# Kernel tuning notes

Measured on AMD Instinct MI355X. Metric: run time of the kernel, lower is better.

The kernel has to match this reference:

```python
import jax, jax.numpy as jnp
import numpy as np

B, T = 1, 1024
HID = 2048
H, HKV, D = 16, 4, 128
G = H // HKV          # kv groups
TOPK = 256
HI, DI = 4, 32        # indexer heads / head dim


def _rotate_half(x):
    x1, x2 = jnp.split(x, 2, axis=-1)
    return jnp.concatenate([-x2, x1], axis=-1)


def _apply_rotary(x, cos, sin):
    # x: (B,T,H,D), cos/sin: (1,T,1,D)
    return x * cos + _rotate_half(x) * sin


def _rms_norm(x):
    eps = jnp.finfo(x.dtype).eps
    return x * jax.lax.rsqrt(jnp.mean(x * x, axis=-1, keepdims=True) + eps)


def setup_inputs() -> dict:
    key = jax.random.key(0)
    ks = jax.random.split(key, 9)
    s = 0.02
    x = jax.random.normal(ks[0], (B, T, HID), jnp.float32)
    # rotary tables
    inv_freq = 1.0 / (10000.0 ** (jnp.arange(0, D, 2, dtype=jnp.float32) / D))
    freqs = jnp.outer(jnp.arange(T, dtype=jnp.float32), inv_freq)   # (T, D/2)
    emb = jnp.concatenate([freqs, freqs], axis=-1)                  # (T, D)
    cos = jnp.cos(emb)[None, :, None, :]
    sin = jnp.sin(emb)[None, :, None, :]
    Wq = jax.random.normal(ks[1], (HID, H * D), jnp.float32) * s
    Wk = jax.random.normal(ks[2], (HID, HKV * D), jnp.float32) * s
    Wv = jax.random.normal(ks[3], (HID, HKV * D), jnp.float32) * s
    Wo = jax.random.normal(ks[4], (H * D, HID), jnp.float32) * s
    Wqi = jax.random.normal(ks[5], (HID, HI * DI), jnp.float32) * s
    Wwi = jax.random.normal(ks[6], (HID, HI), jnp.float32) * s
    Wki = jax.random.normal(ks[7], (HID, DI), jnp.float32) * s
    return {"x": x, "cos": cos, "sin": sin, "Wq": Wq, "Wk": Wk, "Wv": Wv,
            "Wo": Wo, "Wqi": Wqi, "Wwi": Wwi, "Wki": Wki}


def reference(x, cos, sin, Wq, Wk, Wv, Wo, Wqi, Wwi, Wki):
    b, t, _ = x.shape
    q = (x @ Wq).reshape(b, t, H, D)
    k = (x @ Wk).reshape(b, t, HKV, D)
    v = (x @ Wv).reshape(b, t, HKV, D)
    q = _rms_norm(_apply_rotary(q, cos, sin))
    k = _rms_norm(_apply_rotary(k, cos, sin))

    # ---- lightning indexer: I[t,s] = sum_j w[t,j] * relu(q_i[t,j] . k_i[s]) ----
    qi = (x @ Wqi).reshape(b, t, HI, DI)
    wi = x @ Wwi                                   # (B,T,HI)
    ki = x @ Wki                                   # (B,T,DI)
    raw = jax.nn.relu(jnp.einsum('bthd,bsd->bths', qi, ki))
    idx_scores = jnp.einsum('bths,bth->bts', raw, wi)     # (B,T,T)

    pos = jnp.arange(t)
    causal = pos[None, :] <= pos[:, None]                 # (T,T) valid s<=t
    masked = jnp.where(causal[None], idx_scores, -jnp.inf)
    _, top_idx = jax.lax.top_k(masked, TOPK)              # (B,T,K) int32

    # gather selected K/V: (B,T,K,HKV,D)
    gather = jax.vmap(lambda arr, idx: arr[idx])          # per-batch fancy gather
    sel_k = gather(k, top_idx)
    sel_v = gather(v, top_idx)
    sel_mask = top_idx <= pos[None, :, None]              # (B,T,K)

    # grouped-query attention over selected tokens (avoid repeat_interleave)
    q5 = q.reshape(b, t, HKV, G, D)                       # q head h -> kv head h//G
    scale = D ** -0.5
    scores = jnp.einsum('btngd,btknd->btngk', q5, sel_k) * scale
    scores = jnp.where(sel_mask[:, :, None, None, :], scores, -jnp.inf)
    probs = jax.nn.softmax(scores, axis=-1)
    attn = jnp.einsum('btngk,btknd->btngd', probs, sel_v)  # (B,T,HKV,G,D)
    out = attn.reshape(b, t, H * D) @ Wo
    return out
```

## Files before the change

### kernel.cpp

```cpp
#include <hip/hip_runtime.h>
#include <hip/hip_bf16.h>
#include <math.h>

#define T_    1024
#define HID_  2048
#define NH    16
#define NKV   4
#define DH    128
#define TOPK_ 256
#define HI_   4
#define DI_   32
#define NPROJ 3072
#define NIDX  164
#define KSPLIT 8
#define KCHUNK 256

#ifndef INFINITY
#define INFINITY (__builtin_inff())
#endif

typedef __attribute__((ext_vector_type(8))) short bf16x8;
typedef __attribute__((ext_vector_type(4))) float f32x4;

__device__ inline unsigned int packbf(float f) {
    unsigned int u = __float_as_uint(f);
    return (u + 0x7fffu + ((u >> 16) & 1u)) >> 16;
}

#define GLDS16(g, l) __builtin_amdgcn_global_load_lds( \
    (const __attribute__((address_space(1))) void*)(g), \
    (__attribute__((address_space(3))) void*)(l), 16, 0, 0)

__device__ inline void tcast_body(const float* __restrict__ W, unsigned short* __restrict__ Wt,
                                  int N, int bx, int by, int tid, float (*tile)[33]) {
    const int n0 = bx * 32, k0 = by * 32;
    const int tx = tid & 31, ty = tid >> 5;
#pragma unroll
    for (int i = 0; i < 4; ++i)
        tile[ty + i * 8][tx] = W[(size_t)(k0 + ty + i * 8) * N + (n0 + tx)];
    __syncthreads();
#pragma unroll
    for (int i = 0; i < 4; ++i) {
        int n = n0 + ty + i * 8;
        Wt[(size_t)n * HID_ + k0 + tx] = (unsigned short)packbf(tile[tx][ty + i * 8]);
    }
}

__device__ inline void gemm64_body(const unsigned short* __restrict__ A,
                                   const unsigned short* __restrict__ Bt,
                                   float* __restrict__ C, int K, int ldc,
                                   int bx, int by, int tid,
                                   unsigned short* As, unsigned short* Bs) {
    const int lane = tid & 63, w = tid >> 6;
    const int wr = w >> 1, wc = w & 1;
    const int brow = by * 64, bcol = bx * 64;
    const int l15 = lane & 15, lq = lane >> 4;

    f32x4 acc[2][2] = {};

    const int srow = tid >> 3;
    const int gsrc = ((tid & 7) ^ (srow & 7)) * 8;
    const unsigned short* ga  = A  + (size_t)(brow + srow) * K + gsrc;
    const unsigned short* ga2 = ga + (size_t)32 * K;
    const unsigned short* gb  = Bt + (size_t)(bcol + srow) * K + gsrc;
    const unsigned short* gb2 = gb + (size_t)32 * K;
    const int lo1 = tid * 8, lo2 = (tid + 256) * 8;

    GLDS16(ga,  &As[lo1]);
    GLDS16(ga2, &As[lo2]);
    GLDS16(gb,  &Bs[lo1]);
    GLDS16(gb2, &Bs[lo2]);
    __syncthreads();

    const int NT = K >> 6;
    for (int kt = 0; kt < NT; ++kt) {
        const int cur = (kt & 1) * 4096;
        if (kt + 1 < NT) {
            const int nxt = ((kt + 1) & 1) * 4096;
            const int k0 = (kt + 1) << 6;
            GLDS16(ga + k0,  &As[nxt + lo1]);
            GLDS16(ga2 + k0, &As[nxt + lo2]);
            GLDS16(gb + k0,  &Bs[nxt + lo1]);
            GLDS16(gb2 + k0, &Bs[nxt + lo2]);
        }
        const unsigned short* Ac = &As[cur];
        const unsigned short* Bc = &Bs[cur];
        bf16x8 fa[2][2], fb[2][2];
#pragma unroll
        for (int m = 0; m < 2; ++m)
#pragma unroll
            for (int kk = 0; kk < 2; ++kk) {
                int row = wr * 32 + m * 16 + l15;
                fa[m][kk] = *(const bf16x8*)&Ac[row * 64 + (((kk * 4 + lq) ^ (l15 & 7)) * 8)];
            }
#pragma unroll
        for (int nn = 0; nn < 2; ++nn)
#pragma unroll
            for (int kk = 0; kk < 2; ++kk) {
                int row = wc * 32 + nn * 16 + l15;
                fb[nn][kk] = *(const bf16x8*)&Bc[row * 64 + (((kk * 4 + lq) ^ (l15 & 7)) * 8)];
            }
#pragma unroll
        for (int kk = 0; kk < 2; ++kk)
#pragma unroll
            for (int m = 0; m < 2; ++m)
#pragma unroll
                for (int nn = 0; nn < 2; ++nn)
                    acc[m][nn] = __builtin_amdgcn_mfma_f32_16x16x32_bf16(fa[m][kk], fb[nn][kk], acc[m][nn], 0, 0, 0);
        __syncthreads();
    }
#pragma unroll
    for (int m = 0; m < 2; ++m)
#pragma unroll
        for (int nn = 0; nn < 2; ++nn)
#pragma unroll
            for (int q = 0; q < 4; ++q) {
                int row = brow + wr * 32 + m * 16 + lq * 4 + q;
                int col = bcol + wc * 32 + nn * 16 + l15;
                C[(size_t)row * ldc + col] = acc[m][nn][q];
            }
}

__global__ __launch_bounds__(256) void prep1(const float* __restrict__ x,
                                             const float* __restrict__ Wq,
                                             const float* __restrict__ Wk,
                                             const float* __restrict__ Wv,
                                             const float* __restrict__ Wqi,
                                             const float* __restrict__ Wwi,
                                             const float* __restrict__ Wki,
                                             unsigned short* __restrict__ xb,
                                             unsigned short* __restrict__ WtAll,
                                             float* __restrict__ Wi) {
    __shared__ float tile[32][33];
    int bid = blockIdx.x;
    const int tid = threadIdx.x;
    if (bid < 4096) { tcast_body(Wq, WtAll, HID_, bid & 63, bid >> 6, tid, tile); return; }
    bid -= 4096;
    if (bid < 1024) { tcast_body(Wk, WtAll + (size_t)2048 * HID_, 512, bid & 15, bid >> 4, tid, tile); return; }
    bid -= 1024;
    if (bid < 1024) { tcast_body(Wv, WtAll + (size_t)2560 * HID_, 512, bid & 15, bid >> 4, tid, tile); return; }
    bid -= 1024;
    if (bid < 1024) {
        int e = bid * 256 + tid;
        const float4* p = (const float4*)(x + (size_t)e * 8);
        float4 a = p[0], b = p[1];
        uint4 r;
        r.x = packbf(a.x) | (packbf(a.y) << 16);
        r.y = packbf(a.z) | (packbf(a.w) << 16);
        r.z = packbf(b.x) | (packbf(b.y) << 16);
        r.w = packbf(b.z) | (packbf(b.w) << 16);
        *(uint4*)(xb + (size_t)e * 8) = r;
        return;
    }
    bid -= 1024;
    {
        int e = bid * 256 + tid;
        if (e >= HID_ * NIDX) return;
        int k = e / NIDX, c = e - k * NIDX;
        float v;
        if (c < 128) v = Wqi[(size_t)k * 128 + c];
        else if (c < 132) v = Wwi[(size_t)k * 4 + (c - 128)];
        else v = Wki[(size_t)k * 32 + (c - 132)];
        Wi[e] = v;
    }
}

__global__ __launch_bounds__(256) void fusedA(const unsigned short* __restrict__ xb,
                                              const unsigned short* __restrict__ WtAll,
                                              float* __restrict__ proj,
                                              const float* __restrict__ x,
                                              const float* __restrict__ Wi,
                                              float* __restrict__ Cpart,
                                              const float* __restrict__ Wo,
                                              unsigned short* __restrict__ Wot) {
    __shared__ __align__(16) char smem[64 * 64 * 2 * 2 * 2];
    const int tid = threadIdx.x;
    int bid = blockIdx.x;

    if (bid < 768) {
        unsigned short* As = (unsigned short*)smem;
        unsigned short* Bs = As + 8192;
        gemm64_body(xb, WtAll, proj, HID_, NPROJ, bid % 48, bid / 48, tid, As, Bs);
        return;
    }
    bid -= 768;
    if (bid < 384) {
        float (*As2)[68] = (float(*)[68])smem;
        float (*Bs2)[68] = As2 + 16;
        const int bx = bid % 3, by = (bid / 3) % 16, z = bid / 48;
        const int tx = tid & 15, ty = tid >> 4;
        const int brow = by * 64, bcol = bx * 64;
        const int kbeg = z * KCHUNK, kend = kbeg + KCHUNK;
        const int M = T_, N = NIDX, K = HID_;

        const int ar = tid >> 2, ac4 = (tid & 3) * 4;
        const int br = tid >> 4, bc4 = (tid & 15) * 4;

        float acc[4][4];
#pragma unroll
        for (int i = 0; i < 4; ++i)
#pragma unroll
            for (int j = 0; j < 4; ++j) acc[i][j] = 0.f;

        for (int k0 = kbeg; k0 < kend; k0 += 16) {
            float4 va = *(const float4*)&x[(size_t)(brow + ar) * K + k0 + ac4];
            float4 vb;
            int col = bcol + bc4;
            if (col <= N - 4) vb = *(const float4*)&Wi[(size_t)(k0 + br) * N + col];
            else vb = (float4){0.f, 0.f, 0.f, 0.f};
            As2[ac4 + 0][ar] = va.x;
            As2[ac4 + 1][ar] = va.y;
            As2[ac4 + 2][ar] = va.z;
            As2[ac4 + 3][ar] = va.w;
            *(float4*)&Bs2[br][bc4] = vb;
            __syncthreads();
#pragma unroll
            for (int kk = 0; kk < 16; ++kk) {
                float4 a4 = *(const float4*)&As2[kk][ty * 4];
                float4 b4 = *(const float4*)&Bs2[kk][tx * 4];
                float a[4] = {a4.x, a4.y, a4.z, a4.w};
                float b[4] = {b4.x, b4.y, b4.z, b4.w};
#pragma unroll
                for (int i = 0; i < 4; ++i)
#pragma unroll
                    for (int j = 0; j < 4; ++j) acc[i][j] += a[i] * b[j];
            }
            __syncthreads();
        }
#pragma unroll
        for (int i = 0; i < 4; ++i) {
            int r = brow + ty * 4 + i;
#pragma unroll
            for (int j = 0; j < 4; ++j) {
                int c = bcol + tx * 4 + j;
                if (c < NIDX) Cpart[((size_t)z * T_ + r) * NIDX + c] = acc[i][j];
            }
        }
        return;
    }
    bid -= 384;
    {
        float (*tile)[33] = (float(*)[33])smem;
        tcast_body(Wo, Wot, HID_, bid & 63, bid >> 6, tid, tile);
    }
}

__global__ __launch_bounds__(256) void reduce_k(const float* __restrict__ Cpart,
                                                float* __restrict__ Cout,
                                                float* __restrict__ kib, int MN) {
    int e = blockIdx.x * 256 + threadIdx.x;
    if (e >= MN) return;
    float s = 0.f;
#pragma unroll
    for (int z = 0; z < KSPLIT; ++z) s += Cpart[(size_t)z * MN + e];
    Cout[e] = s;
    int t = e / NIDX, c = e - t * NIDX;
    if (c >= 132) kib[(size_t)t * DI_ + (c - 132)] = s;
}

__global__ __launch_bounds__(256) void fusedB(const float* __restrict__ proj,
                                              const float* __restrict__ cosb,
                                              const float* __restrict__ sinb,
                                              unsigned short* __restrict__ qbb,
                                              unsigned short* __restrict__ kbb,
                                              unsigned int* __restrict__ vbb,
                                              const float* __restrict__ proji,
                                              const float* __restrict__ kib,
                                              int* __restrict__ idxout) {
    const int tid = threadIdx.x;
    int bid = blockIdx.x;

    if (bid < 1024) {
        const int t = bid;
        int* orow = idxout + (size_t)t * TOPK_;
        if (t < TOPK_) { orow[tid] = tid; return; }

        __shared__ float qsh[128];
        __shared__ float wsh[4];
        if (tid < 128) qsh[tid] = proji[(size_t)t * NIDX + tid];
        else if (tid < 132) wsh[tid - 128] = proji[(size_t)t * NIDX + tid];
        __syncthreads();

        const int n = t + 1;
        const int lane = tid & 63, wave = tid >> 6;

        unsigned int key[4];
#pragma unroll
        for (int j = 0; j < 4; ++j) {
            int s = j * 256 + tid;
            if (s < n) {
                const float4* kr = (const float4*)&kib[(size_t)s * DI_];
                float4 k4[8];
#pragma unroll
                for (int d4 = 0; d4 < 8; ++d4) k4[d4] = kr[d4];
                float sc = 0.f;
#pragma unroll
                for (int h = 0; h < HI_; ++h) {
                    float d = 0.f;
#pragma unroll
                    for (int d4 = 0; d4 < 8; ++d4) {
                        const float* qp = &qsh[h * 32 + d4 * 4];
                        d += k4[d4].x * qp[0] + k4[d4].y * qp[1] +
                             k4[d4].z * qp[2] + k4[d4].w * qp[3];
                    }
                    sc += wsh[h] * fmaxf(d, 0.f);
                }
                unsigned int u = __float_as_uint(sc);
                key[j] = (u & 0x80000000u) ? ~u : (u | 0x80000000u);
            } else key[j] = 0u;
        }

        __shared__ int wcnt[2][4];
        unsigned int prefix = 0;
#pragma unroll 1
        for (int b = 31; b >= 0; --b) {
            unsigned int cand = prefix | (1u << b);
            int c = (key[0] >= cand) + (key[1] >= cand) + (key[2] >= cand) + (key[3] >= cand);
#pragma unroll
            for (int o = 32; o > 0; o >>= 1) c += __shfl_xor(c, o);
            if (lane == 0) wcnt[b & 1][wave] = c;
            __syncthreads();
            int total = wcnt[b & 1][0] + wcnt[b & 1][1] + wcnt[b & 1][2] + wcnt[b & 1][3];
            if (total >= TOPK_) prefix = cand;
        }
        const unsigned int T = prefix;

        __shared__ int posc;
        __shared__ int eqtot[4][4];
        __syncthreads();
        {
            int c = (key[0] > T) + (key[1] > T) + (key[2] > T) + (key[3] > T);
#pragma unroll
            for (int o = 32; o > 0; o >>= 1) c += __shfl_xor(c, o);
            if (lane == 0) wcnt[0][wave] = c;
        }
        if (tid == 0) posc = 0;

        int e[4]; int myp[4];
#pragma unroll
        for (int j = 0; j < 4; ++j) {
            e[j] = (key[j] == T) ? 1 : 0;
            unsigned long long m = __ballot(e[j]);
            myp[j] = __popcll(m & ((1ull << lane) - 1ull));
            if (lane == 0) eqtot[j][wave] = __popcll(m);
        }
        __syncthreads();
        const int cntGT = wcnt[0][0] + wcnt[0][1] + wcnt[0][2] + wcnt[0][3];
        const int need = TOPK_ - cntGT;

#pragma unroll
        for (int j = 0; j < 4; ++j)
            if (key[j] > T) {
                int p = atomicAdd(&posc, 1);
                orow[p] = j * 256 + tid;
            }
        int runbase = 0;
#pragma unroll
        for (int j = 0; j < 4; ++j) {
            int wavebase = 0;
#pragma unroll
            for (int w2 = 0; w2 < 4; ++w2) if (w2 < wave) wavebase += eqtot[j][w2];
            int g = runbase + wavebase + myp[j];
            if (e[j] && g < need) orow[cntGT + g] = j * 256 + tid;
            runbase += eqtot[j][0] + eqtot[j][1] + eqtot[j][2] + eqtot[j][3];
        }
        return;
    }
    bid -= 1024;
    {
        const int w = tid >> 6, lane = tid & 63;
        const int u = bid * 4 + w;
        const int t = u / 21, h = u - t * 21;
        if (h < 20) {
            const float* row;
            unsigned short* dst;
            if (h < 16) { row = proj + (size_t)t * NPROJ + h * DH;               dst = qbb + ((size_t)t * NH + h) * DH; }
            else        { row = proj + (size_t)t * NPROJ + HID_ + (h - 16) * DH; dst = kbb + ((size_t)t * NKV + (h - 16)) * DH; }
            float a = row[lane], b = row[lane + 64];
            float c0 = cosb[t * DH + lane],      s0 = sinb[t * DH + lane];
            float c1 = cosb[t * DH + lane + 64], s1 = sinb[t * DH + lane + 64];
            float r0 = a * c0 - b * s0;
            float r1 = b * c1 + a * s1;
            float ss = r0 * r0 + r1 * r1;
#pragma unroll
            for (int o = 32; o > 0; o >>= 1) ss += __shfl_xor(ss, o);
            float inv = rsqrtf(ss * (1.0f / 128.0f) + 1.1920929e-07f);
            dst[lane]      = (unsigned short)packbf(r0 * inv);
            dst[lane + 64] = (unsigned short)packbf(r1 * inv);
        } else {
            const float* src = proj + (size_t)t * NPROJ + HID_ + 512;
#pragma unroll
            for (int i = 0; i < 4; ++i) {
                int c2 = lane + i * 64;
                vbb[(size_t)t * 256 + c2] = packbf(src[2 * c2]) | (packbf(src[2 * c2 + 1]) << 16);
            }
        }
    }
}

__global__ __launch_bounds__(256) void gemm64(const unsigned short* __restrict__ A,
                                              const unsigned short* __restrict__ Bt,
                                              float* __restrict__ C,
                                              int K, int ldc) {
    __shared__ unsigned short As[2 * 64 * 64];
    __shared__ unsigned short Bs[2 * 64 * 64];
    gemm64_body(A, Bt, C, K, ldc, blockIdx.x, blockIdx.y, threadIdx.x, As, Bs);
}

__global__ __launch_bounds__(256) void attn8(const unsigned short* __restrict__ qbb,
                                             const unsigned short* __restrict__ kbb,
                                             const unsigned short* __restrict__ vbb,
                                             const int* __restrict__ idx,
                                             unsigned short* __restrict__ attnb) {
    const int t = blockIdx.x, n = blockIdx.y;
    const int tid = threadIdx.x, lane = tid & 63, w = tid >> 6;
    const int C = (t + 1 < TOPK_) ? t + 1 : TOPK_;
    const int l15 = lane & 15, lq = lane >> 4;

    __shared__ int sidx[TOPK_];
    __shared__ float sp[4][TOPK_];
    __shared__ float sinv[4];
    __shared__ unsigned short P[4][264];
    __shared__ unsigned short Vs[2][32 * 128];

    sidx[tid] = idx[(size_t)t * TOPK_ + tid];
    __syncthreads();

#define STAGE_V(buf, tau)                                                          \
    {                                                                              \
        _Pragma("unroll")                                                          \
        for (int it = 0; it < 2; ++it) {                                           \
            int c = tid + it * 256;                                                \
            int r = c >> 4, doff = (c & 15) * 8;                                   \
            int gs = doff ^ (((r >> 3) & 3) << 4);                                 \
            GLDS16(&vbb[((size_t)sidx[(tau) * 32 + r] * NKV + n) * DH + gs],       \
                   &Vs[buf][(size_t)c * 8]);                                       \
        }                                                                          \
    }

    STAGE_V(0, 0);

    const size_t qrow = (size_t)t * NH + n * 4 + (l15 < 4 ? l15 : 3);
    bf16x8 qf[4];
#pragma unroll
    for (int ks = 0; ks < 4; ++ks)
        qf[ks] = *(const bf16x8*)&qbb[qrow * DH + ks * 32 + lq * 8];

    bf16x8 kf[4], kf2[4];
    {
        const unsigned short* kr0 = &kbb[((size_t)sidx[(w * 4) * 16 + l15] * NKV + n) * DH];
#pragma unroll
        for (int ks = 0; ks < 4; ++ks) kf[ks] = *(const bf16x8*)&kr0[ks * 32 + lq * 8];
    }
#pragma unroll
    for (int tt = 0; tt < 4; ++tt) {
        if (tt < 3) {
            const unsigned short* krn =
                &kbb[((size_t)sidx[(w * 4 + tt + 1) * 16 + l15] * NKV + n) * DH];
#pragma unroll
            for (int ks = 0; ks < 4; ++ks) kf2[ks] = *(const bf16x8*)&krn[ks * 32 + lq * 8];
        }
        f32x4 acc = {0.f, 0.f, 0.f, 0.f};
        __builtin_amdgcn_s_setprio(1);
#pragma unroll
        for (int ks = 0; ks < 4; ++ks)
            acc = __builtin_amdgcn_mfma_f32_16x16x32_bf16(qf[ks], kf[ks], acc, 0, 0, 0);
        __builtin_amdgcn_s_setprio(0);
        if (lane < 16) {
            int j = (w * 4 + tt) * 16 + lane;
            bool ok = j < C;
#pragma unroll
            for (int q = 0; q < 4; ++q)
                sp[q][j] = ok ? acc[q] * 0.08838834764831845f : -INFINITY;
        }
#pragma unroll
        for (int ks = 0; ks < 4; ++ks) kf[ks] = kf2[ks];
    }
    __syncthreads();

    {
        float v0 = sp[w][lane], v1 = sp[w][lane + 64],
              v2 = sp[w][lane + 128], v3 = sp[w][lane + 192];
        float m = fmaxf(fmaxf(v0, v1), fmaxf(v2, v3));
#pragma unroll
        for (int o = 32; o > 0; o >>= 1) m = fmaxf(m, __shfl_xor(m, o));
        float e0 = expf(v0 - m), e1 = expf(v1 - m), e2 = expf(v2 - m), e3 = expf(v3 - m);
        float sum = e0 + e1 + e2 + e3;
#pragma unroll
        for (int o = 32; o > 0; o >>= 1) sum += __shfl_xor(sum, o);
        if (lane == 0) sinv[w] = 1.f / sum;
        P[w][lane]       = (unsigned short)packbf(e0);
        P[w][lane + 64]  = (unsigned short)packbf(e1);
        P[w][lane + 128] = (unsigned short)packbf(e2);
        P[w][lane + 192] = (unsigned short)packbf(e3);
    }
    __syncthreads();

    const int prow = (l15 < 4) ? l15 : 3;
    f32x4 pacc[2] = {};
#pragma unroll
    for (int tau = 0; tau < 8; ++tau) {
        const unsigned short* Vb = Vs[tau & 1];
        if (tau < 7) STAGE_V((tau + 1) & 1, tau + 1);
        bf16x8 xf = *(const bf16x8*)&P[prow][tau * 32 + lq * 8];
        const int colr0 = ((2 * w + 0) * 16 + l15) ^ (lq << 4);
        const int colr1 = ((2 * w + 1) * 16 + l15) ^ (lq << 4);
        bf16x8 yf0, yf1;
#pragma unroll
        for (int j = 0; j < 8; ++j) {
            yf0[j] = (short)Vb[(lq * 8 + j) * 128 + colr0];
            yf1[j] = (short)Vb[(lq * 8 + j) * 128 + colr1];
        }
        __builtin_amdgcn_s_setprio(1);
        pacc[0] = __builtin_amdgcn_mfma_f32_16x16x32_bf16(xf, yf0, pacc[0], 0, 0, 0);
        pacc[1] = __builtin_amdgcn_mfma_f32_16x16x32_bf16(xf, yf1, pacc[1], 0, 0, 0);
        __builtin_amdgcn_s_setprio(0);
        __syncthreads();
    }
#undef STAGE_V

    if (lane < 16) {
#pragma unroll
        for (int dt = 0; dt < 2; ++dt)
#pragma unroll
            for (int q = 0; q < 4; ++q)
                attnb[(size_t)(t * NH + n * 4 + q) * DH + (2 * w + dt) * 16 + l15] =
                    (unsigned short)packbf(pacc[dt][q] * sinv[q]);
    }
}

extern "C" void kernel_launch(void* const* d_in, const int* in_sizes, int n_in,
                              void* d_out, int out_size, void* d_ws, size_t ws_size,
                              hipStream_t stream) {
    const float* x    = (const float*)d_in[0];
    const float* cosb = (const float*)d_in[1];
    const float* sinb = (const float*)d_in[2];
    const float* Wq   = (const float*)d_in[3];
    const float* Wk   = (const float*)d_in[4];
    const float* Wv   = (const float*)d_in[5];
    const float* Wo   = (const float*)d_in[6];
    const float* Wqi  = (const float*)d_in[7];
    const float* Wwi  = (const float*)d_in[8];
    const float* Wki  = (const float*)d_in[9];
    float* out = (float*)d_out;

    unsigned short* xb    = (unsigned short*)d_ws;
    unsigned short* WtAll = xb + 2097152;
    float*  proj  = (float*)(WtAll + 6291456);
    float*  Wi    = proj + 3145728;
    float*  proji = Wi + 335872;
    float*  kib   = proji + 167936;
    int*    idxb  = (int*)(kib + 1048576);
    unsigned short* kbb   = (unsigned short*)(idxb + 262144);
    unsigned short* vbb   = kbb + 524288;
    unsigned short* attnb = vbb + 524288;
    unsigned short* Wot   = attnb + 2097152;
    unsigned short* qbb   = xb;
    float* Cpart = (float*)kbb;

    prep1<<<dim3(8480), dim3(256), 0, stream>>>(x, Wq, Wk, Wv, Wqi, Wwi, Wki, xb, WtAll, Wi);

    fusedA<<<dim3(5248), dim3(256), 0, stream>>>(xb, WtAll, proj, x, Wi, Cpart, Wo, Wot);

    reduce_k<<<dim3((T_ * NIDX + 255) / 256), dim3(256), 0, stream>>>(Cpart, proji, kib, T_ * NIDX);

    fusedB<<<dim3(6400), dim3(256), 0, stream>>>(proj, cosb, sinb, qbb, kbb, (unsigned int*)vbb,
                                                 proji, kib, idxb);

    attn8<<<dim3(T_, NKV), dim3(256), 0, stream>>>(qbb, kbb, vbb, idxb, attnb);

    gemm64<<<dim3(HID_ / 64, T_ / 64), dim3(256), 0, stream>>>(attnb, Wot, out, HID_, HID_);
}
```

Before: 151.5 us.

## Split sparse attention over top-k halves with separate softmax combine kernel

Each (token, kv-head) attention block is split into two blocks that each process 128 of the 256 selected keys. Each block writes unnormalized fp32 partial outputs plus per-head max and sum. A new combine kernel merges the halves with log-sum-exp rescaling and writes bf16 output. This doubles parallelism and halves the serial per-block work, at the cost of an extra launch and extra global traffic for the fp32 partials.

```diff
diff --git a/kernel.cpp b/kernel.cpp
--- a/kernel.cpp
+++ b/kernel.cpp
@@ -191,7 +191,7 @@
         const int tx = tid & 15, ty = tid >> 4;
         const int brow = by * 64, bcol = bx * 64;
         const int kbeg = z * KCHUNK, kend = kbeg + KCHUNK;
-        const int M = T_, N = NIDX, K = HID_;
+        const int N = NIDX, K = HID_;
 
         const int ar = tid >> 2, ac4 = (tid & 3) * 4;
         const int br = tid >> 4, bc4 = (tid & 15) * 4;
@@ -407,23 +407,25 @@
     gemm64_body(A, Bt, C, K, ldc, blockIdx.x, blockIdx.y, threadIdx.x, As, Bs);
 }
 
-__global__ __launch_bounds__(256) void attn8(const unsigned short* __restrict__ qbb,
+__global__ __launch_bounds__(256) void attn9(const unsigned short* __restrict__ qbb,
                                              const unsigned short* __restrict__ kbb,
                                              const unsigned short* __restrict__ vbb,
                                              const int* __restrict__ idx,
-                                             unsigned short* __restrict__ attnb) {
-    const int t = blockIdx.x, n = blockIdx.y;
+                                             float* __restrict__ Opart,
+                                             float* __restrict__ mlbuf) {
+    const int t = blockIdx.x;
+    const int n = blockIdx.y >> 1, half = blockIdx.y & 1;
     const int tid = threadIdx.x, lane = tid & 63, w = tid >> 6;
     const int C = (t + 1 < TOPK_) ? t + 1 : TOPK_;
     const int l15 = lane & 15, lq = lane >> 4;
-
-    __shared__ int sidx[TOPK_];
-    __shared__ float sp[4][TOPK_];
-    __shared__ float sinv[4];
-    __shared__ unsigned short P[4][264];
+    const size_t ob = (((size_t)t * NKV + n) * 2 + half) * 4;
+
+    __shared__ int sidx[128];
+    __shared__ float sp[4][128];
+    __shared__ unsigned short P[4][136];
     __shared__ unsigned short Vs[2][32 * 128];
 
-    sidx[tid] = idx[(size_t)t * TOPK_ + tid];
+    if (tid < 128) sidx[tid] = idx[(size_t)t * TOPK_ + half * 128 + tid];
     __syncthreads();
 
 #define STAGE_V(buf, tau)                                                          \
@@ -448,15 +450,15 @@
 
     bf16x8 kf[4], kf2[4];
     {
-        const unsigned short* kr0 = &kbb[((size_t)sidx[(w * 4) * 16 + l15] * NKV + n) * DH];
+        const unsigned short* kr0 = &kbb[((size_t)sidx[(w * 2) * 16 + l15] * NKV + n) * DH];
 #pragma unroll
         for (int ks = 0; ks < 4; ++ks) kf[ks] = *(const bf16x8*)&kr0[ks * 32 + lq * 8];
     }
 #pragma unroll
-    for (int tt = 0; tt < 4; ++tt) {
-        if (tt < 3) {
+    for (int tt = 0; tt < 2; ++tt) {
+        if (tt < 1) {
             const unsigned short* krn =
-                &kbb[((size_t)sidx[(w * 4 + tt + 1) * 16 + l15] * NKV + n) * DH];
+                &kbb[((size_t)sidx[(w * 2 + 1) * 16 + l15] * NKV + n) * DH];
 #pragma unroll
             for (int ks = 0; ks < 4; ++ks) kf2[ks] = *(const bf16x8*)&krn[ks * 32 + lq * 8];
         }
@@ -467,11 +469,11 @@
             acc = __builtin_amdgcn_mfma_f32_16x16x32_bf16(qf[ks], kf[ks], acc, 0, 0, 0);
         __builtin_amdgcn_s_setprio(0);
         if (lane < 16) {
-            int j = (w * 4 + tt) * 16 + lane;
-            bool ok = j < C;
+            int jl = (w * 2 + tt) * 16 + lane;
+            bool ok = (half * 128 + jl) < C;
 #pragma unroll
             for (int q = 0; q < 4; ++q)
-                sp[q][j] = ok ? acc[q] * 0.08838834764831845f : -INFINITY;
+                sp[q][jl] = ok ? acc[q] * 0.08838834764831845f : -INFINITY;
         }
 #pragma unroll
         for (int ks = 0; ks < 4; ++ks) kf[ks] = kf2[ks];
@@ -479,29 +481,30 @@
     __syncthreads();
 
     {
-        float v0 = sp[w][lane], v1 = sp[w][lane + 64],
-              v2 = sp[w][lane + 128], v3 = sp[w][lane + 192];
-        float m = fmaxf(fmaxf(v0, v1), fmaxf(v2, v3));
+        float v0 = sp[w][lane], v1 = sp[w][lane + 64];
+        float m = fmaxf(v0, v1);
 #pragma unroll
         for (int o = 32; o > 0; o >>= 1) m = fmaxf(m, __shfl_xor(m, o));
-        float e0 = expf(v0 - m), e1 = expf(v1 - m), e2 = expf(v2 - m), e3 = expf(v3 - m);
-        float sum = e0 + e1 + e2 + e3;
+        float mg = (m == -INFINITY) ? 0.f : m;
+        float e0 = expf(v0 - mg), e1 = expf(v1 - mg);
+        float sum = e0 + e1;
 #pragma unroll
         for (int o = 32; o > 0; o >>= 1) sum += __shfl_xor(sum, o);
-        if (lane == 0) sinv[w] = 1.f / sum;
-        P[w][lane]       = (unsigned short)packbf(e0);
-        P[w][lane + 64]  = (unsigned short)packbf(e1);
-        P[w][lane + 128] = (unsigned short)packbf(e2);
-        P[w][lane + 192] = (unsigned short)packbf(e3);
+        if (lane == 0) {
+            mlbuf[(ob + w) * 2]     = m;
+            mlbuf[(ob + w) * 2 + 1] = sum;
+        }
+        P[w][lane]      = (unsigned short)packbf(e0);
+        P[w][lane + 64] = (unsigned short)packbf(e1);
     }
     __syncthreads();
 
     const int prow = (l15 < 4) ? l15 : 3;
     f32x4 pacc[2] = {};
 #pragma unroll
-    for (int tau = 0; tau < 8; ++tau) {
+    for (int tau = 0; tau < 4; ++tau) {
         const unsigned short* Vb = Vs[tau & 1];
-        if (tau < 7) STAGE_V((tau + 1) & 1, tau + 1);
+        if (tau < 3) STAGE_V((tau + 1) & 1, tau + 1);
         bf16x8 xf = *(const bf16x8*)&P[prow][tau * 32 + lq * 8];
         const int colr0 = ((2 * w + 0) * 16 + l15) ^ (lq << 4);
         const int colr1 = ((2 * w + 1) * 16 + l15) ^ (lq << 4);
@@ -524,9 +527,28 @@
         for (int dt = 0; dt < 2; ++dt)
 #pragma unroll
             for (int q = 0; q < 4; ++q)
-                attnb[(size_t)(t * NH + n * 4 + q) * DH + (2 * w + dt) * 16 + l15] =
-                    (unsigned short)packbf(pacc[dt][q] * sinv[q]);
-    }
+                Opart[(ob + q) * 128 + (2 * w + dt) * 16 + l15] = pacc[dt][q];
+    }
+}
+
+__global__ __launch_bounds__(256) void attn_combine(const float* __restrict__ Opart,
+                                                    const float* __restrict__ mlbuf,
+                                                    unsigned short* __restrict__ attnb) {
+    const int t = blockIdx.x, n = blockIdx.y;
+    const int tid = threadIdx.x;
+    const int q = tid >> 6, d0 = (tid & 63) * 2;
+    const size_t b0 = (((size_t)t * NKV + n) * 2 + 0) * 4 + q;
+    const size_t b1 = (((size_t)t * NKV + n) * 2 + 1) * 4 + q;
+    float m0 = mlbuf[b0 * 2], l0 = mlbuf[b0 * 2 + 1];
+    float m1 = mlbuf[b1 * 2], l1 = mlbuf[b1 * 2 + 1];
+    float m = fmaxf(m0, m1);
+    float w0 = expf(m0 - m);
+    float w1 = expf(m1 - m);
+    float inv = 1.f / (l0 * w0 + l1 * w1);
+    float o0 = (Opart[b0 * 128 + d0]     * w0 + Opart[b1 * 128 + d0]     * w1) * inv;
+    float o1 = (Opart[b0 * 128 + d0 + 1] * w0 + Opart[b1 * 128 + d0 + 1] * w1) * inv;
+    *(unsigned int*)&attnb[((size_t)t * NH + n * 4 + q) * DH + d0] =
+        packbf(o0) | (packbf(o1) << 16);
 }
 
 extern "C" void kernel_launch(void* const* d_in, const int* in_sizes, int n_in,
@@ -557,6 +579,8 @@
     unsigned short* Wot   = attnb + 2097152;
     unsigned short* qbb   = xb;
     float* Cpart = (float*)kbb;
+    float* Opart = proj;
+    float* mlbuf = proj + 4194304;
 
     prep1<<<dim3(8480), dim3(256), 0, stream>>>(x, Wq, Wk, Wv, Wqi, Wwi, Wki, xb, WtAll, Wi);
 
@@ -567,7 +591,9 @@
     fusedB<<<dim3(6400), dim3(256), 0, stream>>>(proj, cosb, sinb, qbb, kbb, (unsigned int*)vbb,
                                                  proji, kib, idxb);
 
-    attn8<<<dim3(T_, NKV), dim3(256), 0, stream>>>(qbb, kbb, vbb, idxb, attnb);
+    attn9<<<dim3(T_, NKV * 2), dim3(256), 0, stream>>>(qbb, kbb, vbb, idxb, Opart, mlbuf);
+
+    attn_combine<<<dim3(T_, NKV), dim3(256), 0, stream>>>(Opart, mlbuf, attnb);
 
     gemm64<<<dim3(HID_ / 64, T_ / 64), dim3(256), 0, stream>>>(attnb, Wot, out, HID_, HID_);
 }
```

Result: slower. 162.1 us (+7.1%).
